# Optimization experiments

Measured on AMD Instinct MI355X. Metric: run time of the kernel, lower is better.

Reference implementation:

```python
import jax, jax.numpy as jnp
import numpy as np

B, S, E, H, V, C = 64, 512, 256, 128, 50000, 2


def setup_inputs() -> dict:
    key = jax.random.key(0)
    ks = jax.random.split(key, 12)
    sentences = jax.random.randint(ks[0], (B, S), 0, V, dtype=jnp.int32)
    # sparse binary adjacency (dependency-tree-like), float for bmm
    adj = (jax.random.uniform(ks[1], (B, S, S)) < 0.05).astype(jnp.float32)
    emb_table = jax.random.normal(ks[2], (V, E), dtype=jnp.float32) * 0.02
    W1 = jax.random.normal(ks[3], (H, E), dtype=jnp.float32) * 0.05
    b1 = jnp.zeros((H,), jnp.float32)
    W2 = jax.random.normal(ks[4], (H, H), dtype=jnp.float32) * 0.05
    b2 = jnp.zeros((H,), jnp.float32)
    W3 = jax.random.normal(ks[5], (H, H), dtype=jnp.float32) * 0.05
    b3 = jnp.zeros((H,), jnp.float32)
    Wp = jax.random.normal(ks[6], (C, H), dtype=jnp.float32) * 0.05
    bp = jnp.zeros((C,), jnp.float32)
    return {"sentences": sentences, "adj": adj, "emb_table": emb_table,
            "W1": W1, "b1": b1, "W2": W2, "b2": b2, "W3": W3, "b3": b3,
            "Wp": Wp, "bp": bp}


def reference(sentences, adj, emb_table, W1, b1, W2, b2, W3, b3, Wp, bp):
    # embedding lookup (dropout is eval-mode identity)
    h = emb_table[sentences]  # [B, S, E]
    # degree normalization term (self-loop adds +1)
    deg = jnp.sum(adj, axis=-1, keepdims=True) + 1.0  # [B, S, 1]
    for W, b in ((W1, b1), (W2, b2), (W3, b3)):
        agg = jnp.einsum('bst,btd->bsd', adj, h)  # bmm(adj, h)
        # layer(agg) + layer(h) == (agg + h) @ W^T + 2b  (shared weights)
        h = ((agg + h) @ W.T + 2.0 * b) / deg
        h = jax.nn.relu(h)
    # AdaptiveMaxPool1d(1) over sequence dim
    pooled = jnp.max(h, axis=1)  # [B, H]
    logits = pooled @ Wp.T + bp  # [B, C]
    return logits
```

## Files before the change

### kernel.cpp

```cpp
#include <hip/hip_runtime.h>

typedef unsigned short ushort_t;
typedef unsigned long long ull_t;

#define B_ 64
#define S_ 512
#define E_ 256
#define H_ 128
#define M_ (B_ * S_)
#define CAP_ 128

__global__ void k_adjidx(const float* __restrict__ adj,
                         ushort_t* __restrict__ idxl,
                         int* __restrict__ nnz,
                         float* __restrict__ invdeg) {
    int row  = blockIdx.x * 4 + (threadIdx.x >> 6);
    int lane = threadIdx.x & 63;
    const float4* arow = (const float4*)(adj + (size_t)row * S_);
    ushort_t* dst = idxl + (size_t)row * CAP_;
    int total = 0;
    #pragma unroll
    for (int c = 0; c < 2; ++c) {
        float4 v = arow[c * 64 + lane];
        float f[4] = {v.x, v.y, v.z, v.w};
        #pragma unroll
        for (int j = 0; j < 4; ++j) {
            unsigned long long m = __ballot(f[j] != 0.0f);
            if (f[j] != 0.0f) {
                int pos = total + __popcll(m & ((1ull << lane) - 1ull));
                if (pos < CAP_) dst[pos] = (ushort_t)(c * 256 + lane * 4 + j);
            }
            total += __popcll(m);
        }
    }
    if (lane == 0) {
        nnz[row] = total < CAP_ ? total : CAP_;
        invdeg[row] = 1.0f / (float)(total + 1);
    }
}

template <int K, bool GATHER, bool POOL>
__global__ __launch_bounds__(512, 2)
void k_layer(const float* __restrict__ X, const int* __restrict__ sent,
             const float* __restrict__ emb, const float* __restrict__ W,
             const ushort_t* __restrict__ idxl, const int* __restrict__ nnz,
             const float* __restrict__ invdeg, const float* __restrict__ bias,
             float* __restrict__ out) {
    __shared__ __align__(16) float Ys[S_ * 36];
    __shared__ __align__(16) float Xs[2][8 * S_];
    __shared__ __align__(16) float Wsh[2][8 * 32];

    const int tid = threadIdx.x;
    const int bid = blockIdx.x;
    const int xcd = bid & 7, slot = bid >> 3;
    const int b = xcd + 8 * (slot >> 2);
    const int cg = slot & 3;
    const int colBase = cg * 32;
    const int rowBase = b * S_;

    const int r0 = tid >> 1;
    const int kq = (tid & 1) * 4;
    const float* xp0;
    const float* xp1;
    if (GATHER) {
        xp0 = emb + (size_t)sent[rowBase + r0]       * K + kq;
        xp1 = emb + (size_t)sent[rowBase + r0 + 256] * K + kq;
    } else {
        xp0 = X + (size_t)(rowBase + r0)       * K + kq;
        xp1 = X + (size_t)(rowBase + r0 + 256) * K + kq;
    }
    const int wcol = (tid >> 1) & 31;
    const float* wp = W + (size_t)(colBase + wcol) * K + kq;

    const int rg4 = tid & ~3;
    const int c0  = (tid & 3) * 8;

    float acc[4][8] = {};
    float4 g0, g1;
    float4 wv = {0.f, 0.f, 0.f, 0.f};

    constexpr int NC = K / 8;

    g0 = *(const float4*)xp0;
    g1 = *(const float4*)xp1;
    if (tid < 64) wv = *(const float4*)wp;
    Xs[0][(kq + 0) * 512 + r0] = g0.x;
    Xs[0][(kq + 1) * 512 + r0] = g0.y;
    Xs[0][(kq + 2) * 512 + r0] = g0.z;
    Xs[0][(kq + 3) * 512 + r0] = g0.w;
    Xs[0][(kq + 0) * 512 + r0 + 256] = g1.x;
    Xs[0][(kq + 1) * 512 + r0 + 256] = g1.y;
    Xs[0][(kq + 2) * 512 + r0 + 256] = g1.z;
    Xs[0][(kq + 3) * 512 + r0 + 256] = g1.w;
    if (tid < 64) {
        Wsh[0][(kq + 0) * 32 + wcol] = wv.x;
        Wsh[0][(kq + 1) * 32 + wcol] = wv.y;
        Wsh[0][(kq + 2) * 32 + wcol] = wv.z;
        Wsh[0][(kq + 3) * 32 + wcol] = wv.w;
    }
    __syncthreads();

    #pragma unroll 1
    for (int c = 0; c < NC; ++c) {
        const int cur = c & 1;
        if (c + 1 < NC) {
            g0 = *(const float4*)(xp0 + (c + 1) * 8);
            g1 = *(const float4*)(xp1 + (c + 1) * 8);
            if (tid < 64) wv = *(const float4*)(wp + (c + 1) * 8);
        }
        #pragma unroll
        for (int k = 0; k < 8; ++k) {
            const float4 xa = *(const float4*)&Xs[cur][k * 512 + rg4];
            const float4 wa = *(const float4*)&Wsh[cur][k * 32 + c0];
            const float4 wb = *(const float4*)&Wsh[cur][k * 32 + c0 + 4];
            const float xv[4]  = {xa.x, xa.y, xa.z, xa.w};
            const float wv8[8] = {wa.x, wa.y, wa.z, wa.w, wb.x, wb.y, wb.z, wb.w};
            #pragma unroll
            for (int i = 0; i < 4; ++i)
                #pragma unroll
                for (int j = 0; j < 8; ++j)
                    acc[i][j] += xv[i] * wv8[j];
        }
        if (c + 1 < NC) {
            const int nb = cur ^ 1;
            Xs[nb][(kq + 0) * 512 + r0] = g0.x;
            Xs[nb][(kq + 1) * 512 + r0] = g0.y;
            Xs[nb][(kq + 2) * 512 + r0] = g0.z;
            Xs[nb][(kq + 3) * 512 + r0] = g0.w;
            Xs[nb][(kq + 0) * 512 + r0 + 256] = g1.x;
            Xs[nb][(kq + 1) * 512 + r0 + 256] = g1.y;
            Xs[nb][(kq + 2) * 512 + r0 + 256] = g1.z;
            Xs[nb][(kq + 3) * 512 + r0 + 256] = g1.w;
            if (tid < 64) {
                Wsh[nb][(kq + 0) * 32 + wcol] = wv.x;
                Wsh[nb][(kq + 1) * 32 + wcol] = wv.y;
                Wsh[nb][(kq + 2) * 32 + wcol] = wv.z;
                Wsh[nb][(kq + 3) * 32 + wcol] = wv.w;
            }
        }
        __syncthreads();
    }

    #pragma unroll
    for (int i = 0; i < 4; ++i) {
        const int r = rg4 + i;
        *(float4*)&Ys[r * 36 + c0]     = make_float4(acc[i][0], acc[i][1], acc[i][2], acc[i][3]);
        *(float4*)&Ys[r * 36 + c0 + 4] = make_float4(acc[i][4], acc[i][5], acc[i][6], acc[i][7]);
    }
    __syncthreads();

    const int rsub = tid >> 3;
    const int cc   = tid & 7;
    const float4* Ys4 = (const float4*)Ys;
    const float4 bv = *(const float4*)(bias + colBase + cc * 4);
    float4 pmax = {0.f, 0.f, 0.f, 0.f};

    int grow = rowBase + rsub;
    int n_cur = nnz[grow];
    float inv_cur = invdeg[grow];
    const ushort_t* il = idxl + (size_t)grow * CAP_;
    ull_t pk = *(const ull_t*)il;

    #pragma unroll 1
    for (int p = 0; p < 8; ++p) {
        const int r = p * 64 + rsub;
        int n_nxt = 0; float inv_nxt = 0.f; ull_t pk_nxt = 0;
        const ushort_t* il_nxt = il + 64 * CAP_;
        if (p < 7) {
            n_nxt = nnz[grow + 64];
            inv_nxt = invdeg[grow + 64];
            pk_nxt = *(const ull_t*)il_nxt;
        }
        float4 a = Ys4[r * 9 + cc];
        float4 a2 = {0.f, 0.f, 0.f, 0.f};
        const int n = n_cur;
        int i = 0;
        for (; i + 4 <= n; i += 4) {
            const ull_t pk_p = *(const ull_t*)(il + i + 4);
            const int t0 = (int)(pk & 0xffffu);
            const int t1 = (int)((pk >> 16) & 0xffffu);
            const int t2 = (int)((pk >> 32) & 0xffffu);
            const int t3 = (int)((pk >> 48) & 0xffffu);
            const float4 v0 = Ys4[t0 * 9 + cc];
            const float4 v1 = Ys4[t1 * 9 + cc];
            const float4 v2 = Ys4[t2 * 9 + cc];
            const float4 v3 = Ys4[t3 * 9 + cc];
            a.x += v0.x + v1.x;  a.y += v0.y + v1.y;
            a.z += v0.z + v1.z;  a.w += v0.w + v1.w;
            a2.x += v2.x + v3.x; a2.y += v2.y + v3.y;
            a2.z += v2.z + v3.z; a2.w += v2.w + v3.w;
            pk = pk_p;
        }
        for (; i < n; ++i) {
            const int t = il[i];
            const float4 v = Ys4[t * 9 + cc];
            a.x += v.x; a.y += v.y; a.z += v.z; a.w += v.w;
        }
        a.x += a2.x; a.y += a2.y; a.z += a2.z; a.w += a2.w;
        float4 o;
        o.x = fmaxf((a.x + 2.0f * bv.x) * inv_cur, 0.0f);
        o.y = fmaxf((a.y + 2.0f * bv.y) * inv_cur, 0.0f);
        o.z = fmaxf((a.z + 2.0f * bv.z) * inv_cur, 0.0f);
        o.w = fmaxf((a.w + 2.0f * bv.w) * inv_cur, 0.0f);
        if (!POOL) {
            *(float4*)(out + (size_t)(rowBase + r) * H_ + colBase + cc * 4) = o;
        } else {
            pmax.x = fmaxf(pmax.x, o.x); pmax.y = fmaxf(pmax.y, o.y);
            pmax.z = fmaxf(pmax.z, o.z); pmax.w = fmaxf(pmax.w, o.w);
        }
        grow += 64; il = il_nxt;
        n_cur = n_nxt; inv_cur = inv_nxt; pk = pk_nxt;
    }

    if (POOL) {
        float4* smax = (float4*)Xs;
        smax[rsub * 8 + cc] = pmax;
        __syncthreads();
        if (tid < 8) {
            float4 m = smax[tid];
            #pragma unroll 8
            for (int q = 1; q < 64; ++q) {
                const float4 v = smax[q * 8 + tid];
                m.x = fmaxf(m.x, v.x); m.y = fmaxf(m.y, v.y);
                m.z = fmaxf(m.z, v.z); m.w = fmaxf(m.w, v.w);
            }
            *(float4*)(out + (size_t)b * H_ + colBase + tid * 4) = m;
        }
    }
}

__global__ void k_final(const float* __restrict__ pooled,
                        const float* __restrict__ Wp,
                        const float* __restrict__ bp,
                        float* __restrict__ out) {
    int b = blockIdx.x, j = threadIdx.x;
    float m = pooled[(size_t)b * H_ + j];
    float t0 = m * Wp[j];
    float t1 = m * Wp[H_ + j];
    #pragma unroll
    for (int off = 32; off > 0; off >>= 1) {
        t0 += __shfl_down(t0, off);
        t1 += __shfl_down(t1, off);
    }
    __shared__ float red[2][2];
    int wave = j >> 6, lane = j & 63;
    if (lane == 0) { red[0][wave] = t0; red[1][wave] = t1; }
    __syncthreads();
    if (j == 0) out[b * 2 + 0] = red[0][0] + red[0][1] + bp[0];
    if (j == 1) out[b * 2 + 1] = red[1][0] + red[1][1] + bp[1];
}

extern "C" void kernel_launch(void* const* d_in, const int* in_sizes, int n_in,
                              void* d_out, int out_size, void* d_ws, size_t ws_size,
                              hipStream_t stream) {
    const int*   sent = (const int*)d_in[0];
    const float* adj  = (const float*)d_in[1];
    const float* emb  = (const float*)d_in[2];
    const float* W1   = (const float*)d_in[3];
    const float* b1   = (const float*)d_in[4];
    const float* W2   = (const float*)d_in[5];
    const float* b2   = (const float*)d_in[6];
    const float* W3   = (const float*)d_in[7];
    const float* b3   = (const float*)d_in[8];
    const float* Wp   = (const float*)d_in[9];
    const float* bp   = (const float*)d_in[10];
    float* out = (float*)d_out;

    char* ws = (char*)d_ws;
    float*    h1     = (float*)ws;
    float*    h2     = (float*)(ws + ((size_t)16 << 20));
    char*     base   = ws + ((size_t)32 << 20);
    float*    invdeg = (float*)base;
    int*      nnz    = (int*)(base + (size_t)M_ * 4);
    ushort_t* idxl   = (ushort_t*)(base + (size_t)M_ * 8);
    float*    pooled = (float*)(base + (size_t)M_ * 8 + (size_t)M_ * CAP_ * 2);

    k_adjidx<<<M_ / 4, 256, 0, stream>>>(adj, idxl, nnz, invdeg);

    k_layer<E_, true,  false><<<256, 512, 0, stream>>>(nullptr, sent, emb, W1, idxl, nnz, invdeg, b1, h1);
    k_layer<H_, false, false><<<256, 512, 0, stream>>>(h1, nullptr, nullptr, W2, idxl, nnz, invdeg, b2, h2);
    k_layer<H_, false, true ><<<256, 512, 0, stream>>>(h2, nullptr, nullptr, W3, idxl, nnz, invdeg, b3, pooled);

    k_final<<<B_, H_, 0, stream>>>(pooled, Wp, bp, out);
}
```

Baseline: 279.9 us.

## Split layer-2 into separate GEMM and aggregation kernels via global buffer

Refactors the fused layer kernel into phaseA (dense transform) and phaseB (sparse aggregation) device functions. Layer 2 now runs as two kernels that pass the transformed tile through a new global workspace buffer. The phaseB kernel uses only the Ys shared array, so it can fit two blocks per CU. Launch bounds for the fused kernels change from 2 to 1 blocks per CU, and the pooled max reduction becomes a two-stage tree. The split adds a global write and read of the intermediate plus an extra launch.

```diff
diff --git a/kernel.cpp b/kernel.cpp
--- a/kernel.cpp
+++ b/kernel.cpp
@@ -39,25 +39,13 @@
     }
 }
 
-template <int K, bool GATHER, bool POOL>
-__global__ __launch_bounds__(512, 2)
-void k_layer(const float* __restrict__ X, const int* __restrict__ sent,
-             const float* __restrict__ emb, const float* __restrict__ W,
-             const ushort_t* __restrict__ idxl, const int* __restrict__ nnz,
-             const float* __restrict__ invdeg, const float* __restrict__ bias,
-             float* __restrict__ out) {
-    __shared__ __align__(16) float Ys[S_ * 36];
-    __shared__ __align__(16) float Xs[2][8 * S_];
-    __shared__ __align__(16) float Wsh[2][8 * 32];
-
-    const int tid = threadIdx.x;
-    const int bid = blockIdx.x;
-    const int xcd = bid & 7, slot = bid >> 3;
-    const int b = xcd + 8 * (slot >> 2);
-    const int cg = slot & 3;
-    const int colBase = cg * 32;
-    const int rowBase = b * S_;
-
+
+template <int K, bool GATHER>
+__device__ __forceinline__ void phaseA_body(
+        const float* __restrict__ X, const int* __restrict__ sent,
+        const float* __restrict__ emb, const float* __restrict__ W,
+        float* Ys, float (*Xs)[8 * S_], float (*Wsh)[8 * 32],
+        int tid, int colBase, int rowBase) {
     const int r0 = tid >> 1;
     const int kq = (tid & 1) * 4;
     const float* xp0;
@@ -147,8 +135,14 @@
         *(float4*)&Ys[r * 36 + c0]     = make_float4(acc[i][0], acc[i][1], acc[i][2], acc[i][3]);
         *(float4*)&Ys[r * 36 + c0 + 4] = make_float4(acc[i][4], acc[i][5], acc[i][6], acc[i][7]);
     }
-    __syncthreads();
-
+}
+
+template <bool POOL>
+__device__ __forceinline__ void phaseB_body(
+        const ushort_t* __restrict__ idxl, const int* __restrict__ nnz,
+        const float* __restrict__ invdeg, const float* __restrict__ bias,
+        float* __restrict__ out, const float* Ys, float* scratch,
+        int tid, int b, int colBase, int rowBase) {
     const int rsub = tid >> 3;
     const int cc   = tid & 7;
     const float4* Ys4 = (const float4*)Ys;
@@ -203,7 +197,7 @@
         o.z = fmaxf((a.z + 2.0f * bv.z) * inv_cur, 0.0f);
         o.w = fmaxf((a.w + 2.0f * bv.w) * inv_cur, 0.0f);
         if (!POOL) {
-            *(float4*)(out + (size_t)(rowBase + r) * H_ + colBase + cc * 4) = o;
+            ((float4*)(out + (size_t)(rowBase + r) * H_ + colBase))[cc] = o;
         } else {
             pmax.x = fmaxf(pmax.x, o.x); pmax.y = fmaxf(pmax.y, o.y);
             pmax.z = fmaxf(pmax.z, o.z); pmax.w = fmaxf(pmax.w, o.w);
@@ -213,20 +207,113 @@
     }
 
     if (POOL) {
-        float4* smax = (float4*)Xs;
+        float4* smax = (float4*)scratch;
         smax[rsub * 8 + cc] = pmax;
         __syncthreads();
-        if (tid < 8) {
-            float4 m = smax[tid];
-            #pragma unroll 8
-            for (int q = 1; q < 64; ++q) {
-                const float4 v = smax[q * 8 + tid];
+        if (tid < 64) {
+            const int gg = tid >> 3, c2 = tid & 7;
+            float4 m = smax[gg * 8 + c2];
+            #pragma unroll
+            for (int q = 1; q < 8; ++q) {
+                const float4 v = smax[(gg + 8 * q) * 8 + c2];
                 m.x = fmaxf(m.x, v.x); m.y = fmaxf(m.y, v.y);
                 m.z = fmaxf(m.z, v.z); m.w = fmaxf(m.w, v.w);
             }
-            *(float4*)(out + (size_t)b * H_ + colBase + tid * 4) = m;
-        }
-    }
+            smax[512 + gg * 8 + c2] = m;
+        }
+        __syncthreads();
+        if (tid < 8) {
+            float4 m = smax[512 + tid];
+            #pragma unroll
+            for (int g = 1; g < 8; ++g) {
+                const float4 v = smax[512 + g * 8 + tid];
+                m.x = fmaxf(m.x, v.x); m.y = fmaxf(m.y, v.y);
+                m.z = fmaxf(m.z, v.z); m.w = fmaxf(m.w, v.w);
+            }
+            ((float4*)(out + (size_t)b * H_ + colBase))[tid] = m;
+        }
+    }
+}
+
+template <int K, bool GATHER, bool POOL>
+__global__ __launch_bounds__(512, 1)
+void k_layer(const float* __restrict__ X, const int* __restrict__ sent,
+             const float* __restrict__ emb, const float* __restrict__ W,
+             const ushort_t* __restrict__ idxl, const int* __restrict__ nnz,
+             const float* __restrict__ invdeg, const float* __restrict__ bias,
+             float* __restrict__ out) {
+    __shared__ __align__(16) float Ys[S_ * 36];
+    __shared__ __align__(16) float Xs[2][8 * S_];
+    __shared__ __align__(16) float Wsh[2][8 * 32];
+
+    const int tid = threadIdx.x;
+    const int bid = blockIdx.x;
+    const int xcd = bid & 7, slot = bid >> 3;
+    const int b = xcd + 8 * (slot >> 2);
+    const int cg = slot & 3;
+    const int colBase = cg * 32;
+    const int rowBase = b * S_;
+
+    phaseA_body<K, GATHER>(X, sent, emb, W, Ys, Xs, Wsh, tid, colBase, rowBase);
+    __syncthreads();
+    phaseB_body<POOL>(idxl, nnz, invdeg, bias, out, Ys, (float*)Xs,
+                      tid, b, colBase, rowBase);
+}
+
+template <int K>
+__global__ __launch_bounds__(512, 1)
+void k_phaseA(const float* __restrict__ X, const float* __restrict__ W,
+              float* __restrict__ Yb) {
+    __shared__ __align__(16) float Ys[S_ * 36];
+    __shared__ __align__(16) float Xs[2][8 * S_];
+    __shared__ __align__(16) float Wsh[2][8 * 32];
+
+    const int tid = threadIdx.x;
+    const int bid = blockIdx.x;
+    const int xcd = bid & 7, slot = bid >> 3;
+    const int b = xcd + 8 * (slot >> 2);
+    const int cg = slot & 3;
+    const int colBase = cg * 32;
+    const int rowBase = b * S_;
+    (void)b;
+
+    phaseA_body<K, false>(X, nullptr, nullptr, W, Ys, Xs, Wsh, tid, colBase, rowBase);
+    __syncthreads();
+    float4* dst = (float4*)Yb + (size_t)bid * 4096;
+    const float4* Ys4 = (const float4*)Ys;
+    #pragma unroll
+    for (int q = 0; q < 8; ++q) {
+        const int f = q * 512 + tid;
+        dst[f] = Ys4[(f >> 3) * 9 + (f & 7)];
+    }
+}
+
+__global__ __launch_bounds__(512, 2)
+void k_phaseB(const float* __restrict__ Yb,
+              const ushort_t* __restrict__ idxl, const int* __restrict__ nnz,
+              const float* __restrict__ invdeg, const float* __restrict__ bias,
+              float* __restrict__ out) {
+    __shared__ __align__(16) float Ys[S_ * 36];
+
+    const int tid = threadIdx.x;
+    const int bid = blockIdx.x;
+    const int xcd = bid & 7, slot = bid >> 3;
+    const int b = xcd + 8 * (slot >> 2);
+    const int cg = slot & 3;
+    const int colBase = cg * 32;
+    const int rowBase = b * S_;
+
+    const float4* src = (const float4*)Yb + (size_t)bid * 4096;
+    float4* Ys4w = (float4*)Ys;
+    #pragma unroll
+    for (int q = 0; q < 8; ++q) {
+        const int f = q * 512 + tid;
+        Ys4w[(f >> 3) * 9 + (f & 7)] = src[f];
+    }
+    __syncthreads();
+
+    phaseB_body<false>(idxl, nnz, invdeg, bias, out, Ys, nullptr,
+                       tid, b, colBase, rowBase);
 }
 
 __global__ void k_final(const float* __restrict__ pooled,
@@ -269,7 +356,8 @@
     char* ws = (char*)d_ws;
     float*    h1     = (float*)ws;
     float*    h2     = (float*)(ws + ((size_t)16 << 20));
-    char*     base   = ws + ((size_t)32 << 20);
+    float*    Ybuf   = (float*)(ws + ((size_t)32 << 20));
+    char*     base   = ws + ((size_t)48 << 20);
     float*    invdeg = (float*)base;
     int*      nnz    = (int*)(base + (size_t)M_ * 4);
     ushort_t* idxl   = (ushort_t*)(base + (size_t)M_ * 8);
@@ -278,7 +366,8 @@
     k_adjidx<<<M_ / 4, 256, 0, stream>>>(adj, idxl, nnz, invdeg);
 
     k_layer<E_, true,  false><<<256, 512, 0, stream>>>(nullptr, sent, emb, W1, idxl, nnz, invdeg, b1, h1);
-    k_layer<H_, false, false><<<256, 512, 0, stream>>>(h1, nullptr, nullptr, W2, idxl, nnz, invdeg, b2, h2);
+    k_phaseA<H_><<<256, 512, 0, stream>>>(h1, W2, Ybuf);
+    k_phaseB<<<256, 512, 0, stream>>>(Ybuf, idxl, nnz, invdeg, b2, h2);
     k_layer<H_, false, true ><<<256, 512, 0, stream>>>(h2, nullptr, nullptr, W3, idxl, nnz, invdeg, b3, pooled);
 
     k_final<<<B_, H_, 0, stream>>>(pooled, Wp, bp, out);
```

After: 284.2 us. No clear change (+1.6%).

## Fuse all layers into one cooperative persistent kernel with grid syncs

Applied to the files above, without the earlier changes.

Replaces the five separate launches (adjacency indexing, three layers, final projection) with a single cooperative kernel of 256 blocks that steps through the phases, separated by grid-wide barriers. Each block now indexes 128 adjacency rows. The pooling reduction is split into a two-stage tree. This is meant to remove kernel launch gaps and tail effects between stages. In exchange it adds grid.sync costs, allows only one block per CU, and makes the adjacency-indexing phase run on far fewer waves than before.

```diff
diff --git a/kernel.cpp b/kernel.cpp
--- a/kernel.cpp
+++ b/kernel.cpp
@@ -1,4 +1,7 @@
 #include <hip/hip_runtime.h>
+#include <hip/hip_cooperative_groups.h>
+
+namespace cg = cooperative_groups;
 
 typedef unsigned short ushort_t;
 typedef unsigned long long ull_t;
@@ -10,54 +13,12 @@
 #define M_ (B_ * S_)
 #define CAP_ 128
 
-__global__ void k_adjidx(const float* __restrict__ adj,
-                         ushort_t* __restrict__ idxl,
-                         int* __restrict__ nnz,
-                         float* __restrict__ invdeg) {
-    int row  = blockIdx.x * 4 + (threadIdx.x >> 6);
-    int lane = threadIdx.x & 63;
-    const float4* arow = (const float4*)(adj + (size_t)row * S_);
-    ushort_t* dst = idxl + (size_t)row * CAP_;
-    int total = 0;
-    #pragma unroll
-    for (int c = 0; c < 2; ++c) {
-        float4 v = arow[c * 64 + lane];
-        float f[4] = {v.x, v.y, v.z, v.w};
-        #pragma unroll
-        for (int j = 0; j < 4; ++j) {
-            unsigned long long m = __ballot(f[j] != 0.0f);
-            if (f[j] != 0.0f) {
-                int pos = total + __popcll(m & ((1ull << lane) - 1ull));
-                if (pos < CAP_) dst[pos] = (ushort_t)(c * 256 + lane * 4 + j);
-            }
-            total += __popcll(m);
-        }
-    }
-    if (lane == 0) {
-        nnz[row] = total < CAP_ ? total : CAP_;
-        invdeg[row] = 1.0f / (float)(total + 1);
-    }
-}
-
-template <int K, bool GATHER, bool POOL>
-__global__ __launch_bounds__(512, 2)
-void k_layer(const float* __restrict__ X, const int* __restrict__ sent,
-             const float* __restrict__ emb, const float* __restrict__ W,
-             const ushort_t* __restrict__ idxl, const int* __restrict__ nnz,
-             const float* __restrict__ invdeg, const float* __restrict__ bias,
-             float* __restrict__ out) {
-    __shared__ __align__(16) float Ys[S_ * 36];
-    __shared__ __align__(16) float Xs[2][8 * S_];
-    __shared__ __align__(16) float Wsh[2][8 * 32];
-
-    const int tid = threadIdx.x;
-    const int bid = blockIdx.x;
-    const int xcd = bid & 7, slot = bid >> 3;
-    const int b = xcd + 8 * (slot >> 2);
-    const int cg = slot & 3;
-    const int colBase = cg * 32;
-    const int rowBase = b * S_;
-
+template <int K, bool GATHER>
+__device__ __forceinline__ void phaseA_body(
+        const float* __restrict__ X, const int* __restrict__ sent,
+        const float* __restrict__ emb, const float* __restrict__ W,
+        float* Ys, float (*Xs)[8 * S_], float (*Wsh)[8 * 32],
+        int tid, int colBase, int rowBase) {
     const int r0 = tid >> 1;
     const int kq = (tid & 1) * 4;
     const float* xp0;
@@ -147,8 +108,14 @@
         *(float4*)&Ys[r * 36 + c0]     = make_float4(acc[i][0], acc[i][1], acc[i][2], acc[i][3]);
         *(float4*)&Ys[r * 36 + c0 + 4] = make_float4(acc[i][4], acc[i][5], acc[i][6], acc[i][7]);
     }
-    __syncthreads();
-
+}
+
+template <bool POOL>
+__device__ __forceinline__ void phaseB_body(
+        const ushort_t* __restrict__ idxl, const int* __restrict__ nnz,
+        const float* __restrict__ invdeg, const float* __restrict__ bias,
+        float* __restrict__ out, const float* Ys, float* scratch,
+        int tid, int b, int colBase, int rowBase) {
     const int rsub = tid >> 3;
     const int cc   = tid & 7;
     const float4* Ys4 = (const float4*)Ys;
@@ -203,7 +170,7 @@
         o.z = fmaxf((a.z + 2.0f * bv.z) * inv_cur, 0.0f);
         o.w = fmaxf((a.w + 2.0f * bv.w) * inv_cur, 0.0f);
         if (!POOL) {
-            *(float4*)(out + (size_t)(rowBase + r) * H_ + colBase + cc * 4) = o;
+            ((float4*)(out + (size_t)(rowBase + r) * H_ + colBase))[cc] = o;
         } else {
             pmax.x = fmaxf(pmax.x, o.x); pmax.y = fmaxf(pmax.y, o.y);
             pmax.z = fmaxf(pmax.z, o.z); pmax.w = fmaxf(pmax.w, o.w);
@@ -213,41 +180,122 @@
     }
 
     if (POOL) {
-        float4* smax = (float4*)Xs;
+        float4* smax = (float4*)scratch;
         smax[rsub * 8 + cc] = pmax;
         __syncthreads();
-        if (tid < 8) {
-            float4 m = smax[tid];
-            #pragma unroll 8
-            for (int q = 1; q < 64; ++q) {
-                const float4 v = smax[q * 8 + tid];
+        if (tid < 64) {
+            const int gg = tid >> 3, c2 = tid & 7;
+            float4 m = smax[gg * 8 + c2];
+            #pragma unroll
+            for (int q = 1; q < 8; ++q) {
+                const float4 v = smax[(gg + 8 * q) * 8 + c2];
                 m.x = fmaxf(m.x, v.x); m.y = fmaxf(m.y, v.y);
                 m.z = fmaxf(m.z, v.z); m.w = fmaxf(m.w, v.w);
             }
-            *(float4*)(out + (size_t)b * H_ + colBase + tid * 4) = m;
+            smax[512 + gg * 8 + c2] = m;
+        }
+        __syncthreads();
+        if (tid < 8) {
+            float4 m = smax[512 + tid];
+            #pragma unroll
+            for (int g = 1; g < 8; ++g) {
+                const float4 v = smax[512 + g * 8 + tid];
+                m.x = fmaxf(m.x, v.x); m.y = fmaxf(m.y, v.y);
+                m.z = fmaxf(m.z, v.z); m.w = fmaxf(m.w, v.w);
+            }
+            ((float4*)(out + (size_t)b * H_ + colBase))[tid] = m;
         }
     }
 }
 
-__global__ void k_final(const float* __restrict__ pooled,
-                        const float* __restrict__ Wp,
-                        const float* __restrict__ bp,
-                        float* __restrict__ out) {
-    int b = blockIdx.x, j = threadIdx.x;
-    float m = pooled[(size_t)b * H_ + j];
-    float t0 = m * Wp[j];
-    float t1 = m * Wp[H_ + j];
-    #pragma unroll
-    for (int off = 32; off > 0; off >>= 1) {
-        t0 += __shfl_down(t0, off);
-        t1 += __shfl_down(t1, off);
-    }
-    __shared__ float red[2][2];
-    int wave = j >> 6, lane = j & 63;
-    if (lane == 0) { red[0][wave] = t0; red[1][wave] = t1; }
+__global__ __launch_bounds__(512, 1)
+void k_mega(const int* __restrict__ sent, const float* __restrict__ adj,
+            const float* __restrict__ emb,
+            const float* __restrict__ W1, const float* __restrict__ b1,
+            const float* __restrict__ W2, const float* __restrict__ b2,
+            const float* __restrict__ W3, const float* __restrict__ b3,
+            const float* __restrict__ Wp, const float* __restrict__ bp,
+            float* __restrict__ h1, float* __restrict__ h2,
+            ushort_t* __restrict__ idxl, int* __restrict__ nnz,
+            float* __restrict__ invdeg, float* __restrict__ pooled,
+            float* __restrict__ out) {
+    __shared__ __align__(16) float Ys[S_ * 36];
+    __shared__ __align__(16) float Xs[2][8 * S_];
+    __shared__ __align__(16) float Wsh[2][8 * 32];
+
+    cg::grid_group grid = cg::this_grid();
+    const int tid = threadIdx.x;
+    const int bid = blockIdx.x;
+
+    {
+        const int wave = tid >> 6, lane = tid & 63;
+        #pragma unroll 1
+        for (int it = 0; it < 16; ++it) {
+            const int row = bid * 128 + wave * 16 + it;
+            const float4* arow = (const float4*)(adj + (size_t)row * S_);
+            ushort_t* dst = idxl + (size_t)row * CAP_;
+            int total = 0;
+            #pragma unroll
+            for (int c = 0; c < 2; ++c) {
+                float4 v = arow[c * 64 + lane];
+                float f[4] = {v.x, v.y, v.z, v.w};
+                #pragma unroll
+                for (int j = 0; j < 4; ++j) {
+                    unsigned long long m = __ballot(f[j] != 0.0f);
+                    if (f[j] != 0.0f) {
+                        int pos = total + __popcll(m & ((1ull << lane) - 1ull));
+                        if (pos < CAP_) dst[pos] = (ushort_t)(c * 256 + lane * 4 + j);
+                    }
+                    total += __popcll(m);
+                }
+            }
+            if (lane == 0) {
+                nnz[row] = total < CAP_ ? total : CAP_;
+                invdeg[row] = 1.0f / (float)(total + 1);
+            }
+        }
+    }
+    grid.sync();
+
+    const int xcd = bid & 7, slot = bid >> 3;
+    const int b = xcd + 8 * (slot >> 2);
+    const int cgi = slot & 3;
+    const int colBase = cgi * 32;
+    const int rowBase = b * S_;
+
+    phaseA_body<E_, true>(nullptr, sent, emb, W1, Ys, Xs, Wsh, tid, colBase, rowBase);
     __syncthreads();
-    if (j == 0) out[b * 2 + 0] = red[0][0] + red[0][1] + bp[0];
-    if (j == 1) out[b * 2 + 1] = red[1][0] + red[1][1] + bp[1];
+    phaseB_body<false>(idxl, nnz, invdeg, b1, h1, Ys, (float*)Xs, tid, b, colBase, rowBase);
+    grid.sync();
+
+    phaseA_body<H_, false>(h1, nullptr, nullptr, W2, Ys, Xs, Wsh, tid, colBase, rowBase);
+    __syncthreads();
+    phaseB_body<false>(idxl, nnz, invdeg, b2, h2, Ys, (float*)Xs, tid, b, colBase, rowBase);
+    grid.sync();
+
+    phaseA_body<H_, false>(h2, nullptr, nullptr, W3, Ys, Xs, Wsh, tid, colBase, rowBase);
+    __syncthreads();
+    phaseB_body<true>(idxl, nnz, invdeg, b3, pooled, Ys, (float*)Xs, tid, b, colBase, rowBase);
+    grid.sync();
+
+    {
+        const int j = tid & 127;
+        const bool act = (cgi == 0) && (tid < 128);
+        float m  = act ? pooled[(size_t)b * H_ + j] : 0.f;
+        float t0 = act ? m * Wp[j]      : 0.f;
+        float t1 = act ? m * Wp[H_ + j] : 0.f;
+        #pragma unroll
+        for (int off = 32; off > 0; off >>= 1) {
+            t0 += __shfl_down(t0, off);
+            t1 += __shfl_down(t1, off);
+        }
+        __shared__ float red[2][2];
+        const int wave = tid >> 6, lane = tid & 63;
+        if (act && lane == 0) { red[0][wave] = t0; red[1][wave] = t1; }
+        __syncthreads();
+        if (cgi == 0 && tid == 0) out[b * 2 + 0] = red[0][0] + red[0][1] + bp[0];
+        if (cgi == 0 && tid == 1) out[b * 2 + 1] = red[1][0] + red[1][1] + bp[1];
+    }
 }
 
 extern "C" void kernel_launch(void* const* d_in, const int* in_sizes, int n_in,
@@ -275,11 +323,13 @@
     ushort_t* idxl   = (ushort_t*)(base + (size_t)M_ * 8);
     float*    pooled = (float*)(base + (size_t)M_ * 8 + (size_t)M_ * CAP_ * 2);
 
-    k_adjidx<<<M_ / 4, 256, 0, stream>>>(adj, idxl, nnz, invdeg);
-
-    k_layer<E_, true,  false><<<256, 512, 0, stream>>>(nullptr, sent, emb, W1, idxl, nnz, invdeg, b1, h1);
-    k_layer<H_, false, false><<<256, 512, 0, stream>>>(h1, nullptr, nullptr, W2, idxl, nnz, invdeg, b2, h2);
-    k_layer<H_, false, true ><<<256, 512, 0, stream>>>(h2, nullptr, nullptr, W3, idxl, nnz, invdeg, b3, pooled);
-
-    k_final<<<B_, H_, 0, stream>>>(pooled, Wp, bp, out);
+    void* args[] = {
+        (void*)&sent, (void*)&adj, (void*)&emb,
+        (void*)&W1, (void*)&b1, (void*)&W2, (void*)&b2,
+        (void*)&W3, (void*)&b3, (void*)&Wp, (void*)&bp,
+        (void*)&h1, (void*)&h2, (void*)&idxl, (void*)&nnz,
+        (void*)&invdeg, (void*)&pooled, (void*)&out
+    };
+    hipLaunchCooperativeKernel((const void*)k_mega, dim3(256), dim3(512),
+                               args, 0, stream);
 }
```

Result: slower. 421.0 us (+50.4%).
